# Performance work log

Hardware: AMD Instinct MI355X
Metric: run time of the kernel (lower is better)

## Reference

```python
import jax, jax.numpy as jnp
import numpy as np

# dims: S slots, B batch, D pred-rep dim, E slot-embedding dim, H hidden/output dim, V per-slot vocab
S, B, D, E, H, V = 7, 4096, 1024, 128, 512, 200
D0 = D + E  # layer-0 LSTM input size


def setup_inputs() -> dict:
    key = jax.random.key(0)
    ks = jax.random.split(key, 12)
    rn = lambda k, shape, s=0.02: jax.random.normal(k, shape, jnp.float32) * s
    return {
        "pred_reps": jax.random.normal(ks[0], (B, D), jnp.float32),
        "slot_labels": jax.random.randint(ks[1], (S, B), 0, V),
        "emb": rn(ks[2], (S, V, E), 1.0),
        # layer 0: per-slot LSTMCell + highway params
        "Wih0": rn(ks[3], (S, 4 * H, D0)), "Whh0": rn(ks[4], (S, 4 * H, H)),
        "bih0": jnp.zeros((S, 4 * H), jnp.float32), "bhh0": jnp.zeros((S, 4 * H), jnp.float32),
        "hwW0": rn(ks[5], (S, H, D0 + H)), "hwb0": jnp.zeros((S, H), jnp.float32),
        "linW0": rn(ks[6], (S, H, D0)),
        # layer 1 (input size = H)
        "Wih1": rn(ks[7], (S, 4 * H, H)), "Whh1": rn(ks[8], (S, 4 * H, H)),
        "bih1": jnp.zeros((S, 4 * H), jnp.float32), "bhh1": jnp.zeros((S, 4 * H), jnp.float32),
        "hwW1": rn(ks[9], (S, H, 2 * H)), "hwb1": jnp.zeros((S, H), jnp.float32),
        "linW1": rn(ks[10], (S, H, H)),
    }


def _lstm_cell(x, h, c, Wih, Whh, bih, bhh):
    # torch LSTMCell: gates ordered i, f, g, o
    gates = x @ Wih.T + bih + h @ Whh.T + bhh
    i, f, g, o = jnp.split(gates, 4, axis=-1)
    c_new = jax.nn.sigmoid(f) * c + jax.nn.sigmoid(i) * jnp.tanh(g)
    h_new = jax.nn.sigmoid(o) * jnp.tanh(c_new)
    return h_new, c_new


def reference(pred_reps, slot_labels, emb, Wih0, Whh0, bih0, bhh0, hwW0, hwb0, linW0,
              Wih1, Whh1, bih1, bhh1, hwW1, hwb1, linW1):
    def step(carry, xs):
        h0, c0, h1, c1 = carry
        (tbl, idx, wih0, whh0, bi0, bh0, hw0, hb0, lw0,
         wih1, whh1, bi1, bh1, hw1, hb1, lw1) = xs
        # per-slot embedding gather + concat with predicate reps  -> [B, D0]
        x = jnp.concatenate([pred_reps, tbl[idx]], axis=-1)
        # layer 0 cell + highway gate
        h0n, c0n = _lstm_cell(x, h0, c0, wih0, whh0, bi0, bh0)
        gate0 = jax.nn.sigmoid(jnp.concatenate([x, h0n], axis=-1) @ hw0.T + hb0)
        x1 = gate0 * h0n + (1.0 - gate0) * (x @ lw0.T)
        # layer 1 cell (its highway output is dead code in the original: curr_input
        # after the last layer is discarded, so we skip it -- same math)
        h1n, c1n = _lstm_cell(x1, h1, c1, wih1, whh1, bi1, bh1)
        return (h0n, c0n, h1n, c1n), None

    init = tuple(jnp.zeros((B, H), pred_reps.dtype) for _ in range(4))
    xs = (emb, slot_labels, Wih0, Whh0, bih0, bhh0, hwW0, hwb0, linW0,
          Wih1, Whh1, bih1, bhh1, hwW1, hwb1, linW1)
    carry, _ = jax.lax.scan(step, init, xs)
    return carry[2]  # last_h: top-layer hidden after final slot
```

## Files before the change

### kernel.cpp

```cpp
#include <hip/hip_runtime.h>
#include <stdint.h>

typedef unsigned short u16;

#define S_   7
#define B_   4096
#define D_   1024
#define E_   128
#define H_   512
#define V_   200
#define D0_  1152
#define K0_  1664
#define KX1  1024
#define G4H  2048
#define XW   2048
#define X1W  2048

typedef __bf16 bf16x8 __attribute__((ext_vector_type(8)));
typedef float  f32x4  __attribute__((ext_vector_type(4)));
typedef u16    u16x8  __attribute__((ext_vector_type(8)));

__device__ __forceinline__ u16 f2bf(float f) {
  union { float f; uint32_t u; } v; v.f = f;
  uint32_t r = v.u + 0x7fffu + ((v.u >> 16) & 1u);
  return (u16)(r >> 16);
}
__device__ __forceinline__ float bf2f(u16 b) {
  union { uint32_t u; float f; } v; v.u = ((uint32_t)b) << 16;
  return v.f;
}
__device__ __forceinline__ float sigmoidf_(float x) { return 1.0f / (1.0f + __expf(-x)); }
__device__ __forceinline__ float tanhf_(float x) {
  float t = __expf(-2.f * fabsf(x));
  return copysignf((1.f - t) / (1.f + t), x);
}

__device__ __forceinline__ void glds16(const u16* g, u16* l) {
  __builtin_amdgcn_global_load_lds(
      (const __attribute__((address_space(1))) uint32_t*)g,
      (__attribute__((address_space(3))) uint32_t*)l, 16, 0, 0);
}

__device__ __forceinline__ void cvt8s(const float* src, u16* dst) {
  const float4* p = (const float4*)src;
  float4 x = p[0], y = p[1];
  u16x8 o;
  o[0]=f2bf(x.x); o[1]=f2bf(x.y); o[2]=f2bf(x.z); o[3]=f2bf(x.w);
  o[4]=f2bf(y.x); o[5]=f2bf(y.y); o[6]=f2bf(y.z); o[7]=f2bf(y.w);
  *(u16x8*)dst = o;
}

__device__ __forceinline__ void pk_gates(const float* __restrict__ Wih,
                                         const float* __restrict__ Whh,
                                         u16* __restrict__ dst,
                                         int idx, int stride, int NG, int KK,
                                         int P1, int P2, int KA, int KB) {
  #pragma unroll
  for (int u = 0; u < 4; ++u) {
    int i = idx + u * stride;
    int r = i / NG, kg = i - r * NG;
    int k8 = kg * 8;
    int g = r >> 9, j = r & 511;
    long drow = (j >> 4) * 64 + g * 16 + (j & 15);
    const float* sp = (k8 < P1) ? Wih + (long)r * KA + k8
                    : (k8 < P2) ? Whh + (long)r * KB + (k8 - P1)
                                : Wih + (long)r * KA + P1 + (k8 - P2);
    cvt8s(sp, &dst[drow * KK + k8]);
  }
}
__device__ __forceinline__ void pk_hw(const float* __restrict__ src,
                                      u16* __restrict__ dst,
                                      int idx, int stride, int off16, int KS, bool Z2) {
  #pragma unroll
  for (int u = 0; u < 4; ++u) {
    int i = idx + u * stride;
    int r = i / 208, kg = i - r * 208;
    int k8 = kg * 8;
    long drow = ((r & 511) >> 4) * 32 + off16 + (r & 15);
    u16* d = &dst[drow * K0_ + k8];
    if (Z2 && k8 >= 1024 && k8 < 1536) {
      u16x8 z = {};
      *(u16x8*)d = z;
    } else {
      const float* sp = (k8 < 1024) ? src + (long)r * KS + k8
                      : (k8 < 1536) ? src + (long)r * KS + 1152 + (k8 - 1024)
                                    : src + (long)r * KS + 1024 + (k8 - 1536);
      cvt8s(sp, d);
    }
  }
}

__global__ void pack_predz4(const float* __restrict__ pred, u16* __restrict__ dst) {
  const int NG = XW / 8;
  const int stride = gridDim.x * 256;
  int idx = blockIdx.x * 256 + threadIdx.x;
  #pragma unroll
  for (int u = 0; u < 4; ++u) {
    int i = idx + u * stride;
    int row = i / NG, kg = i - row * NG;
    int k8 = kg * 8;
    u16* d = &dst[(long)row * XW + k8];
    if (k8 < 1024) {
      cvt8s(pred + (long)row * D_ + k8, d);
    } else {
      u16x8 z = {};
      *(u16x8*)d = z;
    }
  }
}

__global__ void xgather(const float* __restrict__ emb, const int* __restrict__ labels,
                        u16* __restrict__ EMB) {
  int b = blockIdx.x;
  int e = threadIdx.x;
  #pragma unroll
  for (int s = 0; s < S_; ++s) {
    int ix = labels[s * B_ + b];
    EMB[((long)(s * B_ + b)) * E_ + e] = f2bf(emb[((long)(s * V_ + ix)) * E_ + e]);
  }
}

__global__ void bias_sum(const float* __restrict__ a, const float* __restrict__ b,
                         float* __restrict__ o, int n) {
  int i = blockIdx.x * 256 + threadIdx.x;
  if (i < n) o[i] = a[i] + b[i];
}
__global__ void zero_f(float* __restrict__ p, int n) {
  for (int i = blockIdx.x * 256 + threadIdx.x; i < n; i += gridDim.x * 256) p[i] = 0.f;
}
__global__ void zero_u16k(u16* __restrict__ p, int n) {
  for (int i = blockIdx.x * 256 + threadIdx.x; i < n; i += gridDim.x * 256) p[i] = 0;
}

struct GemmP {
  const u16 *r0, *r1, *r2, *W;
  const float *bsum;
  float *cbuf;
  u16 *hdst;
  float *hf32;
  const u16 *h0src;
  int ld0, ld1, ld2, t1, t2, ldw, nt, ntn, tnw_sh, ncc_sh, tmw, hld, hoff, h0ld, mode;
};
struct PackP {
  const float *wih0, *whh0, *wih1, *whh1, *hww, *linw;
  u16 *wc0, *wc1, *whl;
};

__global__ __launch_bounds__(512, 2)
void gemm_multi(GemmP pa, GemmP pb, GemmP pc, PackP pk, int nA, int nAB, int nABC) {
  const int b   = blockIdx.x;
  const int tid = threadIdx.x;

  if (b >= nABC) {
    int rb = b - nABC;
    if (rb < 208) {
      pk_gates(pk.wih0, pk.whh0, pk.wc0, rb * 512 + tid, 208 * 512,
               208, K0_, 1024, 1536, D0_, H_);
    } else if (rb < 336) {
      pk_gates(pk.wih1, pk.whh1, pk.wc1, (rb - 208) * 512 + tid, 128 * 512,
               128, KX1, 512, 1024, H_, H_);
    } else if (rb < 388) {
      pk_hw(pk.hww,  pk.whl, (rb - 336) * 512 + tid, 52 * 512, 0,  K0_, false);
    } else {
      pk_hw(pk.linw, pk.whl, (rb - 388) * 512 + tid, 52 * 512, 16, D0_, true);
    }
    return;
  }

  __shared__ __align__(16) u16 lds[3 * 16384 + 3 * 8192];
  u16* lA = lds;
  u16* lW = lds + 3 * 16384;

  GemmP P = pc; int base = nAB;
  if (b < nAB) { P = pb; base = nA; }
  if (b < nA)  { P = pa; base = 0; }
  const int bidx = b - base;

  const int lane = tid & 63;
  const int wave = tid >> 6;
  const int xcd = bidx & 7, ci = bidx >> 3;
  const int tn = ((xcd & ((1 << P.ncc_sh) - 1)) << P.tnw_sh) | (ci & ((1 << P.tnw_sh) - 1));
  const int tm = (xcd >> P.ncc_sh) * P.tmw + (ci >> P.tnw_sh);
  const long row0 = (long)tm * 256;
  const long col0 = (long)tn * 128;
  const int wm = (wave >> 1) * 64;
  const int wn = (wave & 1) * 64;
  const int fr = lane & 15;
  const int fk = (lane >> 4) * 8;

  const int srow = wave * 8 + (lane >> 3);
  const int scol = ((lane & 7) ^ ((lane >> 3) & 7)) * 8;
  const u16* gr0 = P.r0 + (row0 + srow) * (long)P.ld0 + scol;
  const u16* gr1 = P.r1 + (row0 + srow) * (long)P.ld1 + scol;
  const u16* gr2 = P.r2 + (row0 + srow) * (long)P.ld2 + scol;
  const u16* gw  = P.W  + (col0 + srow) * (long)P.ldw + scol;
  const int dst0 = wave * 512 + lane * 8;

  auto stage = [&](int t, int buf) {
    const u16* g; long ld;
    if (t < P.t1)      { g = gr0 + (long)t * 64;          ld = P.ld0; }
    else if (t < P.t2) { g = gr1 + (long)(t - P.t1) * 64; ld = P.ld1; }
    else               { g = gr2 + (long)(t - P.t2) * 64; ld = P.ld2; }
    const u16* gww = gw + (long)t * 64;
    u16* dA = lA + buf * 16384 + dst0;
    u16* dW = lW + buf * 8192 + dst0;
    #pragma unroll
    for (int i = 0; i < 4; ++i) glds16(g + (long)(i * 64) * ld, dA + i * 4096);
    #pragma unroll
    for (int j2 = 0; j2 < 2; ++j2) glds16(gww + (long)(j2 * 64) * P.ldw, dW + j2 * 4096);
  };

  int aoff[4], woff[4];
  #pragma unroll
  for (int m = 0; m < 4; ++m) aoff[m] = (wm + m * 16 + fr) * 64;
  #pragma unroll
  for (int n = 0; n < 4; ++n) woff[n] = (wn + n * 16 + fr) * 64;
  const int swz = (fr & 7) << 3;
  const int kk0 = (0 + fk) ^ swz;
  const int kk1 = (32 + fk) ^ swz;

  f32x4 acc[4][4] = {};
  const int nt = P.nt;

  stage(0, 0);
  stage(1, 1);

  for (int t = 0; t < nt; ++t) {
    if (t + 1 < nt) asm volatile("s_waitcnt vmcnt(6)\n\ts_barrier" ::: "memory");
    else            asm volatile("s_waitcnt vmcnt(0)\n\ts_barrier" ::: "memory");
    if (t + 2 < nt) stage(t + 2, (t + 2) % 3);

    const u16* Ab = lA + (t % 3) * 16384;
    const u16* Wb = lW + (t % 3) * 8192;
    bf16x8 af0[4], wf0[4], af1[4], wf1[4];
    #pragma unroll
    for (int m = 0; m < 4; ++m) af0[m] = *(const bf16x8*)&Ab[aoff[m] + kk0];
    #pragma unroll
    for (int n = 0; n < 4; ++n) wf0[n] = *(const bf16x8*)&Wb[woff[n] + kk0];
    #pragma unroll
    for (int m = 0; m < 4; ++m) af1[m] = *(const bf16x8*)&Ab[aoff[m] + kk1];
    #pragma unroll
    for (int n = 0; n < 4; ++n) wf1[n] = *(const bf16x8*)&Wb[woff[n] + kk1];

    __builtin_amdgcn_s_setprio(1);
    #pragma unroll
    for (int m = 0; m < 4; ++m)
      #pragma unroll
      for (int n = 0; n < 4; ++n)
        acc[m][n] = __builtin_amdgcn_mfma_f32_16x16x32_bf16(af0[m], wf0[n], acc[m][n], 0, 0, 0);
    #pragma unroll
    for (int m = 0; m < 4; ++m)
      #pragma unroll
      for (int n = 0; n < 4; ++n)
        acc[m][n] = __builtin_amdgcn_mfma_f32_16x16x32_bf16(af1[m], wf1[n], acc[m][n], 0, 0, 0);
    __builtin_amdgcn_s_setprio(0);
  }

  const int cr = (lane >> 4) * 4;
  const int jg = wn >> 6;

  if (P.mode == 0) {
    const int j = tn * 32 + jg * 16 + fr;
    const float bi = P.bsum[j], bf = P.bsum[512 + j];
    const float bg = P.bsum[1024 + j], bo = P.bsum[1536 + j];
    #pragma unroll
    for (int m = 0; m < 4; ++m) {
      const long rbase = row0 + wm + m * 16 + cr;
      #pragma unroll
      for (int r = 0; r < 4; ++r) {
        const long ri = rbase + r;
        float gi = acc[m][0][r] + bi;
        float gf = acc[m][1][r] + bf;
        float gg = acc[m][2][r] + bg;
        float go = acc[m][3][r] + bo;
        float cv = P.cbuf[ri * H_ + j];
        float cn = sigmoidf_(gf) * cv + sigmoidf_(gi) * tanhf_(gg);
        float hn = sigmoidf_(go) * tanhf_(cn);
        P.cbuf[ri * H_ + j] = cn;
        P.hdst[ri * P.hld + P.hoff + j] = f2bf(hn);
        if (P.hf32) P.hf32[ri * H_ + j] = hn;
      }
    }
  } else {
    #pragma unroll
    for (int pp = 0; pp < 2; ++pp) {
      const int j = tn * 64 + jg * 32 + pp * 16 + fr;
      const float bj = P.bsum[j];
      #pragma unroll
      for (int m = 0; m < 4; ++m) {
        const long rbase = row0 + wm + m * 16 + cr;
        #pragma unroll
        for (int r = 0; r < 4; ++r) {
          const long ri = rbase + r;
          float gv = sigmoidf_(acc[m][2 * pp][r] + bj);
          float h0 = bf2f(P.h0src[ri * (long)P.h0ld + j]);
          float x1 = gv * h0 + (1.f - gv) * acc[m][2 * pp + 1][r];
          P.hdst[ri * P.hld + P.hoff + j] = f2bf(x1);
        }
      }
    }
  }
}

extern "C" void kernel_launch(void* const* d_in, const int* in_sizes, int n_in,
                              void* d_out, int out_size, void* d_ws, size_t ws_size,
                              hipStream_t stream) {
  const float* pred   = (const float*)d_in[0];
  const int*   labels = (const int*)d_in[1];
  const float* emb    = (const float*)d_in[2];
  const float* Wih0   = (const float*)d_in[3];
  const float* Whh0   = (const float*)d_in[4];
  const float* bih0   = (const float*)d_in[5];
  const float* bhh0   = (const float*)d_in[6];
  const float* hwW0   = (const float*)d_in[7];
  const float* hwb0   = (const float*)d_in[8];
  const float* linW0  = (const float*)d_in[9];
  const float* Wih1   = (const float*)d_in[10];
  const float* Whh1   = (const float*)d_in[11];
  const float* bih1   = (const float*)d_in[12];
  const float* bhh1   = (const float*)d_in[13];
  float* out = (float*)d_out;

  char* ws = (char*)d_ws;
  size_t off = 0;
  auto alloc = [&](size_t bytes) {
    char* p = ws + off;
    off = (off + bytes + 255) & ~(size_t)255;
    return p;
  };
  u16* WC0   = (u16*)alloc((size_t)S_ * G4H * K0_ * 2);
  u16* WHLw  = (u16*)alloc((size_t)S_ * 1024 * K0_ * 2);
  u16* WC1   = (u16*)alloc((size_t)S_ * G4H * KX1 * 2);
  u16* xcat  = (u16*)alloc((size_t)B_ * XW * 2);
  u16* EMB   = (u16*)alloc((size_t)S_ * B_ * E_ * 2);
  u16* x1cat = (u16*)alloc((size_t)B_ * X1W * 2);
  float* c0   = (float*)alloc((size_t)B_ * H_ * 4);
  float* c1   = (float*)alloc((size_t)B_ * H_ * 4);
  float* bs0  = (float*)alloc((size_t)S_ * G4H * 4);
  float* bs1  = (float*)alloc((size_t)S_ * G4H * 4);

  auto mkPk = [&](int s) {
    PackP K;
    K.wih0 = Wih0 + (size_t)s * G4H * D0_;
    K.whh0 = Whh0 + (size_t)s * G4H * H_;
    K.wih1 = Wih1 + (size_t)s * G4H * H_;
    K.whh1 = Whh1 + (size_t)s * G4H * H_;
    K.hww  = hwW0 + (size_t)s * H_ * K0_;
    K.linw = linW0 + (size_t)s * H_ * D0_;
    K.wc0  = WC0  + (size_t)s * G4H * K0_;
    K.wc1  = WC1  + (size_t)s * G4H * KX1;
    K.whl  = WHLw + (size_t)s * 1024 * K0_;
    return K;
  };

  GemmP z = {};
  gemm_multi<<<440, 512, 0, stream>>>(z, z, z, mkPk(0), 0, 0, 0);
  pack_predz4<<<1024, 256, 0, stream>>>(pred, xcat);
  xgather<<<B_, E_, 0, stream>>>(emb, labels, EMB);
  bias_sum<<<56, 256, 0, stream>>>(bih0, bhh0, bs0, S_ * G4H);
  bias_sum<<<56, 256, 0, stream>>>(bih1, bhh1, bs1, S_ * G4H);
  zero_f<<<256, 256, 0, stream>>>(c0, B_ * H_);
  zero_f<<<256, 256, 0, stream>>>(c1, B_ * H_);
  zero_u16k<<<2048, 256, 0, stream>>>(x1cat, B_ * X1W);

  auto mkA = [&](int s) {
    GemmP P;
    P.r0 = xcat;                               P.ld0 = XW;  P.t1 = 16;
    P.r1 = xcat + 1024 + ((s + 1) & 1) * 512;  P.ld1 = XW;  P.t2 = 24;
    P.r2 = EMB + (size_t)s * B_ * E_;          P.ld2 = E_;
    P.W = WC0 + (size_t)s * G4H * K0_;         P.ldw = K0_; P.nt = 26;
    P.ntn = 16; P.tnw_sh = 3; P.ncc_sh = 1; P.tmw = 4;
    P.bsum = bs0 + (size_t)s * G4H; P.cbuf = c0;
    P.hdst = xcat; P.hld = XW; P.hoff = 1024 + (s & 1) * 512;
    P.hf32 = nullptr; P.h0src = xcat; P.h0ld = 0; P.mode = 0;
    return P;
  };
  auto mkB = [&](int s) {
    GemmP P;
    P.r0 = xcat;                               P.ld0 = XW;  P.t1 = 16;
    P.r1 = xcat + 1024 + (s & 1) * 512;        P.ld1 = XW;  P.t2 = 24;
    P.r2 = EMB + (size_t)s * B_ * E_;          P.ld2 = E_;
    P.W = WHLw + (size_t)s * 1024 * K0_;       P.ldw = K0_; P.nt = 26;
    P.ntn = 8; P.tnw_sh = 2; P.ncc_sh = 1; P.tmw = 4;
    P.bsum = hwb0 + (size_t)s * H_; P.cbuf = nullptr;
    P.hdst = x1cat; P.hld = X1W; P.hoff = (s & 1) * 512;
    P.hf32 = nullptr;
    P.h0src = xcat + 1024 + (s & 1) * 512; P.h0ld = XW; P.mode = 1;
    return P;
  };
  auto mkC = [&](int s) {
    GemmP P;
    P.r0 = x1cat + (s & 1) * 512;              P.ld0 = X1W; P.t1 = 8;
    P.r1 = x1cat + 1024 + ((s + 1) & 1) * 512; P.ld1 = X1W; P.t2 = 16;
    P.r2 = P.r0;                               P.ld2 = X1W;
    P.W = WC1 + (size_t)s * G4H * KX1;         P.ldw = KX1; P.nt = 16;
    P.ntn = 16; P.tnw_sh = 3; P.ncc_sh = 1; P.tmw = 4;
    P.bsum = bs1 + (size_t)s * G4H; P.cbuf = c1;
    P.hdst = x1cat; P.hld = X1W; P.hoff = 1024 + (s & 1) * 512;
    P.hf32 = (s == 6) ? out : nullptr; P.h0src = x1cat; P.h0ld = 0; P.mode = 0;
    return P;
  };

  for (int k = 0; k <= 8; ++k) {
    const int nA = (k <= 6) ? 256 : 0;
    const int nB = (k >= 1 && k <= 7) ? 128 : 0;
    const int nC = (k >= 2) ? 256 : 0;
    const int nD = (k <= 5) ? 440 : 0;
    GemmP pa, pb, pc;
    if (nA) pa = mkA(k);
    if (nB) pb = mkB(k - 1);
    if (nC) pc = mkC(k - 2);
    GemmP any = nA ? pa : (nB ? pb : pc);
    if (!nA) pa = any;
    if (!nB) pb = any;
    if (!nC) pc = any;
    PackP pk = mkPk(nD ? (k + 1) : 0);
    gemm_multi<<<nA + nB + nC + nD, 512, 0, stream>>>(pa, pb, pc, pk,
                                                      nA, nA + nB, nA + nB + nC);
  }
}
```

Measured before the change: 626.6 us.

## Split GEMM k-step into four phases interleaving LDS reads, global prefetch, and MFMAs

Restructures the main GEMM loop so each k-tile is processed in four sub-phases. Each phase loads a 2x2 quadrant of fragments from LDS, issues one quarter of the next-next tile's global-to-LDS copies, and runs that quadrant's MFMAs. Barriers and explicit waitcnts are placed between phases. This spreads memory traffic across the MFMA stream for better overlap, in a ping-pong style. The cost is many more barriers per tile and repeated fragment reloads, since the A fragments are reread per n-half and the W fragments per m-half.

```diff
diff --git a/kernel.cpp b/kernel.cpp
--- a/kernel.cpp
+++ b/kernel.cpp
@@ -196,11 +196,14 @@
   const u16* gw  = P.W  + (col0 + srow) * (long)P.ldw + scol;
   const int dst0 = wave * 512 + lane * 8;
 
+  auto asrc = [&](int t, const u16** g, long* ld) {
+    if (t < P.t1)      { *g = gr0 + (long)t * 64;          *ld = P.ld0; }
+    else if (t < P.t2) { *g = gr1 + (long)(t - P.t1) * 64; *ld = P.ld1; }
+    else               { *g = gr2 + (long)(t - P.t2) * 64; *ld = P.ld2; }
+  };
   auto stage = [&](int t, int buf) {
     const u16* g; long ld;
-    if (t < P.t1)      { g = gr0 + (long)t * 64;          ld = P.ld0; }
-    else if (t < P.t2) { g = gr1 + (long)(t - P.t1) * 64; ld = P.ld1; }
-    else               { g = gr2 + (long)(t - P.t2) * 64; ld = P.ld2; }
+    asrc(t, &g, &ld);
     const u16* gww = gw + (long)t * 64;
     u16* dA = lA + buf * 16384 + dst0;
     u16* dW = lW + buf * 8192 + dst0;
@@ -209,6 +212,19 @@
     #pragma unroll
     for (int j2 = 0; j2 < 2; ++j2) glds16(gww + (long)(j2 * 64) * P.ldw, dW + j2 * 4096);
   };
+  auto stage_part = [&](int t, int buf, int q) {
+    u16* dA = lA + buf * 16384 + dst0;
+    u16* dW = lW + buf * 8192 + dst0;
+    if (q < 2) {
+      const u16* g; long ld;
+      asrc(t, &g, &ld);
+      glds16(g + (long)((2 * q) * 64) * ld,     dA + (2 * q) * 4096);
+      glds16(g + (long)((2 * q + 1) * 64) * ld, dA + (2 * q + 1) * 4096);
+    } else {
+      const u16* gww = gw + (long)t * 64;
+      glds16(gww + (long)((q - 2) * 64) * P.ldw, dW + (q - 2) * 4096);
+    }
+  };
 
   int aoff[4], woff[4];
   #pragma unroll
@@ -223,37 +239,49 @@
   const int nt = P.nt;
 
   stage(0, 0);
-  stage(1, 1);
+  if (nt > 1) stage(1, 1);
+  if (nt > 1) asm volatile("s_waitcnt vmcnt(6)" ::: "memory");
+  else        asm volatile("s_waitcnt vmcnt(0)" ::: "memory");
+  __builtin_amdgcn_s_barrier();
 
   for (int t = 0; t < nt; ++t) {
-    if (t + 1 < nt) asm volatile("s_waitcnt vmcnt(6)\n\ts_barrier" ::: "memory");
-    else            asm volatile("s_waitcnt vmcnt(0)\n\ts_barrier" ::: "memory");
-    if (t + 2 < nt) stage(t + 2, (t + 2) % 3);
-
     const u16* Ab = lA + (t % 3) * 16384;
     const u16* Wb = lW + (t % 3) * 8192;
-    bf16x8 af0[4], wf0[4], af1[4], wf1[4];
     #pragma unroll
-    for (int m = 0; m < 4; ++m) af0[m] = *(const bf16x8*)&Ab[aoff[m] + kk0];
-    #pragma unroll
-    for (int n = 0; n < 4; ++n) wf0[n] = *(const bf16x8*)&Wb[woff[n] + kk0];
-    #pragma unroll
-    for (int m = 0; m < 4; ++m) af1[m] = *(const bf16x8*)&Ab[aoff[m] + kk1];
-    #pragma unroll
-    for (int n = 0; n < 4; ++n) wf1[n] = *(const bf16x8*)&Wb[woff[n] + kk1];
-
-    __builtin_amdgcn_s_setprio(1);
-    #pragma unroll
-    for (int m = 0; m < 4; ++m)
+    for (int q = 0; q < 4; ++q) {
+      const int mh = q >> 1, nh = q & 1;
+      bf16x8 af0[2], af1[2], wf0[2], wf1[2];
       #pragma unroll
-      for (int n = 0; n < 4; ++n)
-        acc[m][n] = __builtin_amdgcn_mfma_f32_16x16x32_bf16(af0[m], wf0[n], acc[m][n], 0, 0, 0);
-    #pragma unroll
-    for (int m = 0; m < 4; ++m)
+      for (int mm = 0; mm < 2; ++mm) {
+        af0[mm] = *(const bf16x8*)&Ab[aoff[2 * mh + mm] + kk0];
+        af1[mm] = *(const bf16x8*)&Ab[aoff[2 * mh + mm] + kk1];
+      }
       #pragma unroll
-      for (int n = 0; n < 4; ++n)
-        acc[m][n] = __builtin_amdgcn_mfma_f32_16x16x32_bf16(af1[m], wf1[n], acc[m][n], 0, 0, 0);
-    __builtin_amdgcn_s_setprio(0);
+      for (int nn = 0; nn < 2; ++nn) {
+        wf0[nn] = *(const bf16x8*)&Wb[woff[2 * nh + nn] + kk0];
+        wf1[nn] = *(const bf16x8*)&Wb[woff[2 * nh + nn] + kk1];
+      }
+      if (t + 2 < nt) stage_part(t + 2, (t + 2) % 3, q);
+      __builtin_amdgcn_s_barrier();
+      asm volatile("s_waitcnt lgkmcnt(0)" ::: "memory");
+      __builtin_amdgcn_sched_barrier(0);
+      __builtin_amdgcn_s_setprio(1);
+      #pragma unroll
+      for (int mm = 0; mm < 2; ++mm)
+        #pragma unroll
+        for (int nn = 0; nn < 2; ++nn) {
+          acc[2 * mh + mm][2 * nh + nn] = __builtin_amdgcn_mfma_f32_16x16x32_bf16(
+              af0[mm], wf0[nn], acc[2 * mh + mm][2 * nh + nn], 0, 0, 0);
+          acc[2 * mh + mm][2 * nh + nn] = __builtin_amdgcn_mfma_f32_16x16x32_bf16(
+              af1[mm], wf1[nn], acc[2 * mh + mm][2 * nh + nn], 0, 0, 0);
+        }
+      __builtin_amdgcn_s_setprio(0);
+      if (q == 3 && t + 1 < nt) {
+        if (t + 2 < nt) asm volatile("s_waitcnt vmcnt(6)" ::: "memory");
+        else            asm volatile("s_waitcnt vmcnt(0)" ::: "memory");
+      }
+      __builtin_amdgcn_s_barrier();
+    }
   }
 
   const int cr = (lane >> 4) * 4;
```

Result: slower. 944.0 us (+50.7%).

## Split highway/linear GEMMs, shrink tiles to 128x128 with 256-thread double buffering

Applied to the files above, without the earlier changes.

Reworks the fused GEMM kernel to use 128x128 tiles with 256 threads and a double-buffered LDS pipeline in place of the earlier 256x128, 512-thread triple-buffered one. The combined highway+linear weight matrix is split in two. The linear projection x@linW.T now runs as its own GEMM over the real K=1152, written to a bf16 buffer, and the highway GEMM reads that buffer in its epilogue. This drops the zero-padded K columns from the linear part and frees the highway GEMM from needing paired accumulators. The costs are more blocks, less reuse per tile, an extra bf16 round-trip for the linear output, and the loss of the setprio and the deeper prefetch.

```diff
diff --git a/kernel.cpp b/kernel.cpp
--- a/kernel.cpp
+++ b/kernel.cpp
@@ -11,6 +11,7 @@
 #define V_   200
 #define D0_  1152
 #define K0_  1664
+#define KL_  1152
 #define KX1  1024
 #define G4H  2048
 #define XW   2048
@@ -68,25 +69,29 @@
     cvt8s(sp, &dst[drow * KK + k8]);
   }
 }
-__device__ __forceinline__ void pk_hw(const float* __restrict__ src,
-                                      u16* __restrict__ dst,
-                                      int idx, int stride, int off16, int KS, bool Z2) {
+__device__ __forceinline__ void pk_hwn(const float* __restrict__ src,
+                                       u16* __restrict__ dst,
+                                       int idx, int stride) {
   #pragma unroll
   for (int u = 0; u < 4; ++u) {
     int i = idx + u * stride;
     int r = i / 208, kg = i - r * 208;
     int k8 = kg * 8;
-    long drow = ((r & 511) >> 4) * 32 + off16 + (r & 15);
-    u16* d = &dst[drow * K0_ + k8];
-    if (Z2 && k8 >= 1024 && k8 < 1536) {
-      u16x8 z = {};
-      *(u16x8*)d = z;
-    } else {
-      const float* sp = (k8 < 1024) ? src + (long)r * KS + k8
-                      : (k8 < 1536) ? src + (long)r * KS + 1152 + (k8 - 1024)
-                                    : src + (long)r * KS + 1024 + (k8 - 1536);
-      cvt8s(sp, d);
-    }
+    const float* sp = (k8 < 1024) ? src + (long)r * K0_ + k8
+                    : (k8 < 1536) ? src + (long)r * K0_ + 1152 + (k8 - 1024)
+                                  : src + (long)r * K0_ + 1024 + (k8 - 1536);
+    cvt8s(sp, &dst[(long)r * K0_ + k8]);
+  }
+}
+__device__ __forceinline__ void pk_lin(const float* __restrict__ src,
+                                       u16* __restrict__ dst,
+                                       int idx, int stride) {
+  #pragma unroll
+  for (int u = 0; u < 4; ++u) {
+    int i = idx + u * stride;
+    int r = i / 144, kg = i - r * 144;
+    int k8 = kg * 8;
+    cvt8s(src + (long)r * KL_ + k8, &dst[(long)r * KL_ + k8]);
   }
 }
 
@@ -139,62 +144,65 @@
   u16 *hdst;
   float *hf32;
   const u16 *h0src;
-  int ld0, ld1, ld2, t1, t2, ldw, nt, ntn, tnw_sh, ncc_sh, tmw, hld, hoff, h0ld, mode;
+  const u16 *xsrc;
+  int ld0, ld1, ld2, t1, t2, ldw, nt, ntn, cpx, hld, hoff, h0ld, xld, mode;
 };
 struct PackP {
   const float *wih0, *whh0, *wih1, *whh1, *hww, *linw;
-  u16 *wc0, *wc1, *whl;
+  u16 *wc0, *wc1, *whn, *wln;
 };
 
-__global__ __launch_bounds__(512, 2)
-void gemm_multi(GemmP pa, GemmP pb, GemmP pc, PackP pk, int nA, int nAB, int nABC) {
+__global__ __launch_bounds__(256)
+void gemm_multi(GemmP pa, GemmP pb, GemmP pl, GemmP pc, PackP pk,
+                int nA, int nAB, int nABL, int nABLC) {
   const int b   = blockIdx.x;
   const int tid = threadIdx.x;
 
-  if (b >= nABC) {
-    int rb = b - nABC;
-    if (rb < 208) {
-      pk_gates(pk.wih0, pk.whh0, pk.wc0, rb * 512 + tid, 208 * 512,
+  if (b >= nABLC) {
+    int rb = b - nABLC;
+    if (rb < 416) {
+      pk_gates(pk.wih0, pk.whh0, pk.wc0, rb * 256 + tid, 416 * 256,
                208, K0_, 1024, 1536, D0_, H_);
-    } else if (rb < 336) {
-      pk_gates(pk.wih1, pk.whh1, pk.wc1, (rb - 208) * 512 + tid, 128 * 512,
+    } else if (rb < 672) {
+      pk_gates(pk.wih1, pk.whh1, pk.wc1, (rb - 416) * 256 + tid, 256 * 256,
                128, KX1, 512, 1024, H_, H_);
-    } else if (rb < 388) {
-      pk_hw(pk.hww,  pk.whl, (rb - 336) * 512 + tid, 52 * 512, 0,  K0_, false);
+    } else if (rb < 776) {
+      pk_hwn(pk.hww, pk.whn, (rb - 672) * 256 + tid, 104 * 256);
     } else {
-      pk_hw(pk.linw, pk.whl, (rb - 388) * 512 + tid, 52 * 512, 16, D0_, true);
+      pk_lin(pk.linw, pk.wln, (rb - 776) * 256 + tid, 72 * 256);
     }
     return;
   }
 
-  __shared__ __align__(16) u16 lds[3 * 16384 + 3 * 8192];
+  __shared__ __align__(16) u16 lds[4 * 8192];
+  GemmP P = pc; int base = nABL;
+  if (b < nABL) { P = pl; base = nAB; }
+  if (b < nAB)  { P = pb; base = nA; }
+  if (b < nA)   { P = pa; base = 0; }
+  const int bidx = b - base;
+
   u16* lA = lds;
-  u16* lW = lds + 3 * 16384;
-
-  GemmP P = pc; int base = nAB;
-  if (b < nAB) { P = pb; base = nA; }
-  if (b < nA)  { P = pa; base = 0; }
-  const int bidx = b - base;
-
+  u16* lW = lds + 2 * 8192;
   const int lane = tid & 63;
   const int wave = tid >> 6;
-  const int xcd = bidx & 7, ci = bidx >> 3;
-  const int tn = ((xcd & ((1 << P.ncc_sh) - 1)) << P.tnw_sh) | (ci & ((1 << P.tnw_sh) - 1));
-  const int tm = (xcd >> P.ncc_sh) * P.tmw + (ci >> P.tnw_sh);
-  const long row0 = (long)tm * 256;
+  const int bid  = (bidx & 7) * P.cpx + (bidx >> 3);
+  const int tn = bid % P.ntn;
+  const int tm = bid / P.ntn;
+  const long row0 = (long)tm * 128;
   const long col0 = (long)tn * 128;
   const int wm = (wave >> 1) * 64;
   const int wn = (wave & 1) * 64;
   const int fr = lane & 15;
   const int fk = (lane >> 4) * 8;
-
-  const int srow = wave * 8 + (lane >> 3);
+  const int wr = wave * 32;
+
+  const int srow = wr + (lane >> 3);
   const int scol = ((lane & 7) ^ ((lane >> 3) & 7)) * 8;
   const u16* gr0 = P.r0 + (row0 + srow) * (long)P.ld0 + scol;
   const u16* gr1 = P.r1 + (row0 + srow) * (long)P.ld1 + scol;
   const u16* gr2 = P.r2 + (row0 + srow) * (long)P.ld2 + scol;
   const u16* gw  = P.W  + (col0 + srow) * (long)P.ldw + scol;
-  const int dst0 = wave * 512 + lane * 8;
+  const int dst0 = wr * 64 + lane * 8;
 
   auto stage = [&](int t, int buf) {
     const u16* g; long ld;
@@ -202,12 +210,13 @@
     else if (t < P.t2) { g = gr1 + (long)(t - P.t1) * 64; ld = P.ld1; }
     else               { g = gr2 + (long)(t - P.t2) * 64; ld = P.ld2; }
     const u16* gww = gw + (long)t * 64;
-    u16* dA = lA + buf * 16384 + dst0;
+    u16* dA = lA + buf * 8192 + dst0;
     u16* dW = lW + buf * 8192 + dst0;
     #pragma unroll
-    for (int i = 0; i < 4; ++i) glds16(g + (long)(i * 64) * ld, dA + i * 4096);
-    #pragma unroll
-    for (int j2 = 0; j2 < 2; ++j2) glds16(gww + (long)(j2 * 64) * P.ldw, dW + j2 * 4096);
+    for (int i = 0; i < 4; ++i) {
+      glds16(g   + (long)(i * 8) * ld,    dA + i * 512);
+      glds16(gww + (long)(i * 8) * P.ldw, dW + i * 512);
+    }
   };
 
   int aoff[4], woff[4];
@@ -223,15 +232,12 @@
   const int nt = P.nt;
 
   stage(0, 0);
-  stage(1, 1);
 
   for (int t = 0; t < nt; ++t) {
-    if (t + 1 < nt) asm volatile("s_waitcnt vmcnt(6)\n\ts_barrier" ::: "memory");
-    else            asm volatile("s_waitcnt vmcnt(0)\n\ts_barrier" ::: "memory");
-    if (t + 2 < nt) stage(t + 2, (t + 2) % 3);
-
-    const u16* Ab = lA + (t % 3) * 16384;
-    const u16* Wb = lW + (t % 3) * 8192;
+    __syncthreads();
+    if (t + 1 < nt) stage(t + 1, (t + 1) & 1);
+    const u16* Ab = lA + (t & 1) * 8192;
+    const u16* Wb = lW + (t & 1) * 8192;
     bf16x8 af0[4], wf0[4], af1[4], wf1[4];
     #pragma unroll
     for (int m = 0; m < 4; ++m) af0[m] = *(const bf16x8*)&Ab[aoff[m] + kk0];
@@ -241,8 +247,6 @@
     for (int m = 0; m < 4; ++m) af1[m] = *(const bf16x8*)&Ab[aoff[m] + kk1];
     #pragma unroll
     for (int n = 0; n < 4; ++n) wf1[n] = *(const bf16x8*)&Wb[woff[n] + kk1];
-
-    __builtin_amdgcn_s_setprio(1);
     #pragma unroll
     for (int m = 0; m < 4; ++m)
       #pragma unroll
@@ -253,7 +257,6 @@
       #pragma unroll
       for (int n = 0; n < 4; ++n)
         acc[m][n] = __builtin_amdgcn_mfma_f32_16x16x32_bf16(af1[m], wf1[n], acc[m][n], 0, 0, 0);
-    __builtin_amdgcn_s_setprio(0);
   }
 
   const int cr = (lane >> 4) * 4;
@@ -281,10 +284,10 @@
         if (P.hf32) P.hf32[ri * H_ + j] = hn;
       }
     }
-  } else {
-    #pragma unroll
-    for (int pp = 0; pp < 2; ++pp) {
-      const int j = tn * 64 + jg * 32 + pp * 16 + fr;
+  } else if (P.mode == 1) {
+    #pragma unroll
+    for (int n = 0; n < 4; ++n) {
+      const int j = (int)(col0) + wn + n * 16 + fr;
       const float bj = P.bsum[j];
       #pragma unroll
       for (int m = 0; m < 4; ++m) {
@@ -292,11 +295,24 @@
         #pragma unroll
         for (int r = 0; r < 4; ++r) {
           const long ri = rbase + r;
-          float gv = sigmoidf_(acc[m][2 * pp][r] + bj);
+          float gv = sigmoidf_(acc[m][n][r] + bj);
           float h0 = bf2f(P.h0src[ri * (long)P.h0ld + j]);
-          float x1 = gv * h0 + (1.f - gv) * acc[m][2 * pp + 1][r];
+          float xl = bf2f(P.xsrc[ri * (long)P.xld + j]);
+          float x1 = gv * h0 + (1.f - gv) * xl;
           P.hdst[ri * P.hld + P.hoff + j] = f2bf(x1);
         }
+      }
+    }
+  } else {
+    #pragma unroll
+    for (int n = 0; n < 4; ++n) {
+      const int j = (int)(col0) + wn + n * 16 + fr;
+      #pragma unroll
+      for (int m = 0; m < 4; ++m) {
+        const long rbase = row0 + wm + m * 16 + cr;
+        #pragma unroll
+        for (int r = 0; r < 4; ++r)
+          P.hdst[(rbase + r) * P.hld + P.hoff + j] = f2bf(acc[m][n][r]);
       }
     }
   }
@@ -328,16 +344,18 @@
     off = (off + bytes + 255) & ~(size_t)255;
     return p;
   };
-  u16* WC0   = (u16*)alloc((size_t)S_ * G4H * K0_ * 2);
-  u16* WHLw  = (u16*)alloc((size_t)S_ * 1024 * K0_ * 2);
-  u16* WC1   = (u16*)alloc((size_t)S_ * G4H * KX1 * 2);
-  u16* xcat  = (u16*)alloc((size_t)B_ * XW * 2);
-  u16* EMB   = (u16*)alloc((size_t)S_ * B_ * E_ * 2);
-  u16* x1cat = (u16*)alloc((size_t)B_ * X1W * 2);
-  float* c0   = (float*)alloc((size_t)B_ * H_ * 4);
-  float* c1   = (float*)alloc((size_t)B_ * H_ * 4);
-  float* bs0  = (float*)alloc((size_t)S_ * G4H * 4);
-  float* bs1  = (float*)alloc((size_t)S_ * G4H * 4);
+  u16* WC0  = (u16*)alloc((size_t)S_ * G4H * K0_ * 2);
+  u16* WC1  = (u16*)alloc((size_t)S_ * G4H * KX1 * 2);
+  u16* HWn  = (u16*)alloc((size_t)S_ * H_ * K0_ * 2);
+  u16* LNw  = (u16*)alloc((size_t)S_ * H_ * KL_ * 2);
+  u16* xcat = (u16*)alloc((size_t)B_ * XW * 2);
+  u16* EMB  = (u16*)alloc((size_t)S_ * B_ * E_ * 2);
+  u16* x1cat= (u16*)alloc((size_t)B_ * X1W * 2);
+  u16* xlin = (u16*)alloc((size_t)2 * B_ * H_ * 2);
+  float* c0  = (float*)alloc((size_t)B_ * H_ * 4);
+  float* c1  = (float*)alloc((size_t)B_ * H_ * 4);
+  float* bs0 = (float*)alloc((size_t)S_ * G4H * 4);
+  float* bs1 = (float*)alloc((size_t)S_ * G4H * 4);
 
   auto mkPk = [&](int s) {
     PackP K;
@@ -346,15 +364,16 @@
     K.wih1 = Wih1 + (size_t)s * G4H * H_;
     K.whh1 = Whh1 + (size_t)s * G4H * H_;
     K.hww  = hwW0 + (size_t)s * H_ * K0_;
-    K.linw = linW0 + (size_t)s * H_ * D0_;
-    K.wc0  = WC0  + (size_t)s * G4H * K0_;
-    K.wc1  = WC1  + (size_t)s * G4H * KX1;
-    K.whl  = WHLw + (size_t)s * 1024 * K0_;
+    K.linw = linW0 + (size_t)s * H_ * KL_;
+    K.wc0  = WC0 + (size_t)s * G4H * K0_;
+    K.wc1  = WC1 + (size_t)s * G4H * KX1;
+    K.whn  = HWn + (size_t)s * H_ * K0_;
+    K.wln  = LNw + (size_t)s * H_ * KL_;
     return K;
   };
 
   GemmP z = {};
-  gemm_multi<<<440, 512, 0, stream>>>(z, z, z, mkPk(0), 0, 0, 0);
+  gemm_multi<<<848, 256, 0, stream>>>(z, z, z, z, mkPk(0), 0, 0, 0, 0);
   pack_predz4<<<1024, 256, 0, stream>>>(pred, xcat);
   xgather<<<B_, E_, 0, stream>>>(emb, labels, EMB);
   bias_sum<<<56, 256, 0, stream>>>(bih0, bhh0, bs0, S_ * G4H);
@@ -364,58 +383,79 @@
   zero_u16k<<<2048, 256, 0, stream>>>(x1cat, B_ * X1W);
 
   auto mkA = [&](int s) {
-    GemmP P;
+    GemmP P = {};
     P.r0 = xcat;                               P.ld0 = XW;  P.t1 = 16;
     P.r1 = xcat + 1024 + ((s + 1) & 1) * 512;  P.ld1 = XW;  P.t2 = 24;
     P.r2 = EMB + (size_t)s * B_ * E_;          P.ld2 = E_;
     P.W = WC0 + (size_t)s * G4H * K0_;         P.ldw = K0_; P.nt = 26;
-    P.ntn = 16; P.tnw_sh = 3; P.ncc_sh = 1; P.tmw = 4;
+    P.ntn = 16; P.cpx = 64;
     P.bsum = bs0 + (size_t)s * G4H; P.cbuf = c0;
     P.hdst = xcat; P.hld = XW; P.hoff = 1024 + (s & 1) * 512;
-    P.hf32 = nullptr; P.h0src = xcat; P.h0ld = 0; P.mode = 0;
+    P.hf32 = nullptr; P.h0src = xcat; P.h0ld = 0; P.xsrc = xcat; P.xld = 0;
+    P.mode = 0;
     return P;
   };
   auto mkB = [&](int s) {
-    GemmP P;
+    GemmP P = {};
     P.r0 = xcat;                               P.ld0 = XW;  P.t1 = 16;
     P.r1 = xcat + 1024 + (s & 1) * 512;        P.ld1 = XW;  P.t2 = 24;
     P.r2 = EMB + (size_t)s * B_ * E_;          P.ld2 = E_;
-    P.W = WHLw + (size_t)s * 1024 * K0_;       P.ldw = K0_; P.nt = 26;
-    P.ntn = 8; P.tnw_sh = 2; P.ncc_sh = 1; P.tmw = 4;
+    P.W = HWn + (size_t)s * H_ * K0_;          P.ldw = K0_; P.nt = 26;
+    P.ntn = 4; P.cpx = 16;
     P.bsum = hwb0 + (size_t)s * H_; P.cbuf = nullptr;
     P.hdst = x1cat; P.hld = X1W; P.hoff = (s & 1) * 512;
     P.hf32 = nullptr;
-    P.h0src = xcat + 1024 + (s & 1) * 512; P.h0ld = XW; P.mode = 1;
+    P.h0src = xcat + 1024 + (s & 1) * 512; P.h0ld = XW;
+    P.xsrc = xlin + (size_t)(s & 1) * B_ * H_; P.xld = H_;
+    P.mode = 1;
     return P;
   };
+  auto mkL = [&](int s) {
+    GemmP P = {};
+    P.r0 = xcat;                               P.ld0 = XW;  P.t1 = 16;
+    P.r1 = xcat;                               P.ld1 = XW;  P.t2 = 16;
+    P.r2 = EMB + (size_t)s * B_ * E_;          P.ld2 = E_;
+    P.W = LNw + (size_t)s * H_ * KL_;          P.ldw = KL_; P.nt = 18;
+    P.ntn = 4; P.cpx = 16;
+    P.bsum = hwb0; P.cbuf = nullptr;
+    P.hdst = xlin + (size_t)(s & 1) * B_ * H_; P.hld = H_; P.hoff = 0;
+    P.hf32 = nullptr; P.h0src = xcat; P.h0ld = 0; P.xsrc = xcat; P.xld = 0;
+    P.mode = 2;
+    return P;
+  };
   auto mkC = [&](int s) {
-    GemmP P;
+    GemmP P = {};
     P.r0 = x1cat + (s & 1) * 512;              P.ld0 = X1W; P.t1 = 8;
     P.r1 = x1cat + 1024 + ((s + 1) & 1) * 512; P.ld1 = X1W; P.t2 = 16;
     P.r2 = P.r0;                               P.ld2 = X1W;
     P.W = WC1 + (size_t)s * G4H * KX1;         P.ldw = KX1; P.nt = 16;
-    P.ntn = 16; P.tnw_sh = 3; P.ncc_sh = 1; P.tmw = 4;
+    P.ntn = 16; P.cpx = 64;
     P.bsum = bs1 + (size_t)s * G4H; P.cbuf = c1;
     P.hdst = x1cat; P.hld = X1W; P.hoff = 1024 + (s & 1) * 512;
-    P.hf32 = (s == 6) ? out : nullptr; P.h0src = x1cat; P.h0ld = 0; P.mode = 0;
+    P.hf32 = (s == 6) ? out : nullptr; P.h0src = x1cat; P.h0ld = 0;
+    P.xsrc = x1cat; P.xld = 0;
+    P.mode = 0;
     return P;
   };
 
   for (int k = 0; k <= 8; ++k) {
-    const int nA = (k <= 6) ? 256 : 0;
+    const int nA = (k <= 6) ? 512 : 0;
     const int nB = (k >= 1 && k <= 7) ? 128 : 0;
-    const int nC = (k >= 2) ? 256 : 0;
-    const int nD = (k <= 5) ? 440 : 0;
-    GemmP pa, pb, pc;
+    const int nL = (k <= 6) ? 128 : 0;
+    const int nC = (k >= 2) ? 512 : 0;
+    const int nD = (k <= 5) ? 848 : 0;
+    GemmP pa, pb, pl, pc;
     if (nA) pa = mkA(k);
     if (nB) pb = mkB(k - 1);
+    if (nL) pl = mkL(k);
     if (nC) pc = mkC(k - 2);
-    GemmP any = nA ? pa : (nB ? pb : pc);
+    GemmP any = nA ? pa : (nB ? pb : (nL ? pl : pc));
     if (!nA) pa = any;
     if (!nB) pb = any;
+    if (!nL) pl = any;
     if (!nC) pc = any;
     PackP pk = mkPk(nD ? (k + 1) : 0);
-    gemm_multi<<<nA + nB + nC + nD, 512, 0, stream>>>(pa, pb, pc, pk,
-                                                      nA, nA + nB, nA + nB + nC);
-  }
-}
+    gemm_multi<<<nA + nB + nL + nC + nD, 256, 0, stream>>>(
+        pa, pb, pl, pc, pk, nA, nA + nB, nA + nB + nL, nA + nB + nL + nC);
+  }
+}
```

Result: no change. 630.9 us (+0.7%).
